# Performance work log

Hardware: AMD Instinct MI355X
Metric: run time of the kernel (lower is better)

The kernel has to match this reference:

```python
import jax, jax.numpy as jnp
import numpy as np

C = 256
HEADS = 8
HD = C // HEADS
WS = 7
SCALE = HD ** -0.5
EPS = 1e-5


def _ln(x, g, b):
    m = jnp.mean(x, axis=-1, keepdims=True)
    v = jnp.var(x, axis=-1, keepdims=True)
    return (x - m) * jax.lax.rsqrt(v + EPS) * g + b


def setup_inputs() -> dict:
    key = jax.random.key(0)
    ks = jax.random.split(key, 8)
    B, H, W = 32, 56, 56
    N = H * W
    hid = 4 * C
    s = lambda fan: 1.0 / np.sqrt(fan)
    return {
        "x": jax.random.normal(ks[0], (B, N, C), dtype=jnp.float32),
        "ln1_g": jnp.ones((C,), jnp.float32),
        "ln1_b": jnp.zeros((C,), jnp.float32),
        "qkv_w": jax.random.normal(ks[1], (C, 3 * C), jnp.float32) * s(C),
        "qkv_b": jnp.zeros((3 * C,), jnp.float32),
        "ln2_g": jnp.ones((C,), jnp.float32),
        "ln2_b": jnp.zeros((C,), jnp.float32),
        "fc1_w": jax.random.normal(ks[2], (C, hid), jnp.float32) * s(C),
        "fc1_b": jnp.zeros((hid,), jnp.float32),
        "mlp_ln_g": jnp.ones((hid,), jnp.float32),
        "mlp_ln_b": jnp.zeros((hid,), jnp.float32),
        "fc2_w": jax.random.normal(ks[3], (hid, C), jnp.float32) * s(hid),
        "fc2_b": jnp.zeros((C,), jnp.float32),
        "H": H,
        "W": W,
    }


def _lsa(x, qkv_w, qkv_b, H, W):
    # x: (B, N, C); H, W divisible by WS -> padding is zero (matches torch path)
    B, N, _ = x.shape
    hp, wp = H // WS, W // WS
    P = hp * wp
    # window partition: (B, P, WS*WS, C)
    xw = x.reshape(B, hp, WS, wp, WS, C).transpose(0, 1, 3, 2, 4, 5).reshape(B, P, WS * WS, C)
    qkv = xw @ qkv_w + qkv_b                      # (B, P, 49, 3C)
    qkv = qkv.reshape(B, P, WS * WS, 3, HEADS, HD).transpose(3, 0, 1, 4, 2, 5)
    q, k, v = qkv[0], qkv[1], qkv[2]              # (B, P, heads, 49, HD)
    attn = jax.nn.softmax(jnp.einsum('bphqd,bphkd->bphqk', q * SCALE, k), axis=-1)
    out = jnp.einsum('bphqk,bphkd->bphqd', attn, v)
    # merge heads, un-window: note LSA never applies self.proj (faithful)
    out = out.transpose(0, 1, 3, 2, 4).reshape(B, hp, wp, WS, WS, C)
    out = out.transpose(0, 1, 3, 2, 4, 5).reshape(B, N, C)
    return out


def reference(x, ln1_g, ln1_b, qkv_w, qkv_b, ln2_g, ln2_b,
              fc1_w, fc1_b, mlp_ln_g, mlp_ln_b, fc2_w, fc2_b, H, W):
    x = x + _lsa(_ln(x, ln1_g, ln1_b), qkv_w, qkv_b, H, W)
    h = _ln(x, ln2_g, ln2_b)
    h = jax.nn.gelu(h @ fc1_w + fc1_b, approximate=False)
    h = _ln(h, mlp_ln_g, mlp_ln_b)
    x = x + (h @ fc2_w + fc2_b)
    return x
```

## Files before the change

### kernel.cpp

```cpp
#include <hip/hip_runtime.h>
#include <cmath>

typedef __bf16 bf16;
typedef __bf16 bf16x4 __attribute__((ext_vector_type(4)));
typedef __bf16 bf16x8 __attribute__((ext_vector_type(8)));
typedef float floatx4 __attribute__((ext_vector_type(4)));

constexpr int BATCH = 32;
constexpr int NTOK  = 3136;
constexpr int CDIM  = 256;
constexpr int MROWS = BATCH * NTOK;
constexpr int HIDD  = 1024;
constexpr float ATTN_SCALE = 0.17677669529663689f;

__device__ __forceinline__ float gelu_fast(float x) {
    float p = fmaf(0.044715f * x, x * x, x);
    return __fdividef(x, 1.0f + __expf(-1.5957691216057308f * p));
}

__device__ __forceinline__ void load8(const bf16* p, float* o) {
    bf16x8 v = *reinterpret_cast<const bf16x8*>(p);
#pragma unroll
    for (int j = 0; j < 8; j++) o[j] = (float)v[j];
}

__device__ __forceinline__ void gload_lds16(const void* g, void* l) {
    __builtin_amdgcn_global_load_lds(
        (const __attribute__((address_space(1))) void*)g,
        (__attribute__((address_space(3))) void*)l, 16, 0, 0);
}

__global__ __launch_bounds__(256) void wt_kernel(
    const float* __restrict__ Win, bf16* __restrict__ Wt, int Ksz, int Nsz,
    const float* __restrict__ gsc, int swz)
{
    int id = blockIdx.x * 256 + threadIdx.x;
    int n = id / Ksz, k = id % Ksz;
    float v = Win[(size_t)k * Nsz + n];
    if (gsc) v *= gsc[k];
    int kp = k ^ (swz & ((n & 7) << 3));
    Wt[(size_t)n * Ksz + kp] = (bf16)v;
}

__global__ __launch_bounds__(256) void c12_part_kernel(
    const float* __restrict__ W, const float* __restrict__ g,
    const float* __restrict__ b, float2* __restrict__ part)
{
    int n = threadIdx.x, j = blockIdx.x;
    float c1 = 0.f, c2 = 0.f;
#pragma unroll 8
    for (int k = j * 64; k < j * 64 + 64; k++) {
        float w = W[(size_t)k * 256 + n];
        c1 = fmaf(b[k], w, c1);
        c2 = fmaf(g[k], w, c2);
    }
    part[j * 256 + n] = make_float2(c1, c2);
}

__global__ __launch_bounds__(256) void c12_red_kernel(
    const float2* __restrict__ part, float2* __restrict__ c12)
{
    int n = threadIdx.x;
    float c1 = 0.f, c2 = 0.f;
#pragma unroll
    for (int j = 0; j < 16; j++) { float2 p = part[j * 256 + n]; c1 += p.x; c2 += p.y; }
    c12[n] = make_float2(c1, c2);
}

__global__ __launch_bounds__(256) void ln_apply_f32_kernel(
    const float* __restrict__ X, const float* __restrict__ g,
    const float* __restrict__ b, bf16* __restrict__ Y, int swz)
{
    int tok  = (blockIdx.x * 256 + threadIdx.x) >> 6;
    int lane = threadIdx.x & 63;
    const float* row = X + (size_t)tok * CDIM;
    float4 v = *reinterpret_cast<const float4*>(row + lane * 4);
    float s  = v.x + v.y + v.z + v.w;
    float ss = v.x * v.x + v.y * v.y + v.z * v.z + v.w * v.w;
#pragma unroll
    for (int off = 32; off > 0; off >>= 1) {
        s  += __shfl_xor(s,  off, 64);
        ss += __shfl_xor(ss, off, 64);
    }
    float mean = s * (1.0f / CDIM);
    float var  = ss * (1.0f / CDIM) - mean * mean;
    if (var < 0.f) var = 0.f;
    float rstd = rsqrtf(var + 1e-5f);
    float4 gg = *reinterpret_cast<const float4*>(g + lane * 4);
    float4 bb = *reinterpret_cast<const float4*>(b + lane * 4);
    bf16x4 o;
    o[0] = (bf16)((v.x - mean) * rstd * gg.x + bb.x);
    o[1] = (bf16)((v.y - mean) * rstd * gg.y + bb.y);
    o[2] = (bf16)((v.z - mean) * rstd * gg.z + bb.z);
    o[3] = (bf16)((v.w - mean) * rstd * gg.w + bb.w);
    int off4 = (lane * 4) ^ (swz & ((tok & 7) << 3));
    *reinterpret_cast<bf16x4*>(Y + (size_t)tok * CDIM + off4) = o;
}

__global__ __launch_bounds__(256) void ln_inplace_h_kernel(
    bf16* __restrict__ H, const float* __restrict__ g, const float* __restrict__ b)
{
    int tok  = (blockIdx.x * 256 + threadIdx.x) >> 6;
    int lane = threadIdx.x & 63;
    bf16* row = H + (size_t)tok * HIDD;
    float f[16];
    load8(row + lane * 8, f);
    load8(row + 512 + lane * 8, f + 8);
    float s = 0.f, ss = 0.f;
#pragma unroll
    for (int j = 0; j < 16; j++) { s += f[j]; ss += f[j] * f[j]; }
#pragma unroll
    for (int off = 32; off > 0; off >>= 1) {
        s  += __shfl_xor(s,  off, 64);
        ss += __shfl_xor(ss, off, 64);
    }
    float mean = s * (1.0f / HIDD);
    float var  = ss * (1.0f / HIDD) - mean * mean;
    if (var < 0.f) var = 0.f;
    float rstd = rsqrtf(var + 1e-5f);
    bf16x8 o0, o1;
#pragma unroll
    for (int j = 0; j < 8; j++) {
        o0[j] = (bf16)((f[j]     - mean) * rstd * g[lane * 8 + j]       + b[lane * 8 + j]);
        o1[j] = (bf16)((f[j + 8] - mean) * rstd * g[512 + lane * 8 + j] + b[512 + lane * 8 + j]);
    }
    *reinterpret_cast<bf16x8*>(row + lane * 8) = o0;
    *reinterpret_cast<bf16x8*>(row + 512 + lane * 8) = o1;
}

template<int EPI, bool SWZ, typename TO>
__global__ __launch_bounds__(256) void gemm_bt_kernel(
    const bf16* __restrict__ A, const bf16* __restrict__ Bt,
    const float* __restrict__ bias, const float* __restrict__ resid,
    TO* __restrict__ out, int Nsz, int Ksz)
{
    __shared__ bf16 lA[128 * 64];
    __shared__ bf16 lB[128 * 64];
    const int t = threadIdx.x;
    const int lane = t & 63, w = t >> 6;
    const int quad = lane >> 4, l16 = lane & 15;
    const int wm = (w >> 1) * 64, wn = (w & 1) * 64;

    const int gx   = gridDim.x;
    const int flat = blockIdx.y * gx + blockIdx.x;
    const int cpx  = (gx * gridDim.y) >> 3;
    const int fl2  = (flat & 7) * cpx + (flat >> 3);
    const int bx   = fl2 % gx, by = fl2 / gx;

    const size_t m0 = (size_t)by * 128;
    const int n0 = bx * 128;
    const int srow = w * 32 + (lane >> 3);
    const int scol = (lane & 7) * 8;
    const int swzr = SWZ ? ((l16 & 7) << 3) : 0;

    floatx4 acc[4][4] = {};

    for (int kc = 0; kc < Ksz; kc += 64) {
#pragma unroll
        for (int j = 0; j < 4; j++) {
            gload_lds16(A  + (m0 + srow + j * 8) * Ksz + kc + scol, &lA[(w * 32 + j * 8) * 64]);
            gload_lds16(Bt + (size_t)(n0 + srow + j * 8) * Ksz + kc + scol, &lB[(w * 32 + j * 8) * 64]);
        }
        __syncthreads();
#pragma unroll
        for (int ks = 0; ks < 64; ks += 32) {
            bf16x8 af[4], bfv[4];
#pragma unroll
            for (int i = 0; i < 4; i++) {
                af[i]  = *reinterpret_cast<const bf16x8*>(&lA[(wm + i * 16 + l16) * 64 + ((ks + quad * 8) ^ swzr)]);
                bfv[i] = *reinterpret_cast<const bf16x8*>(&lB[(wn + i * 16 + l16) * 64 + ((ks + quad * 8) ^ swzr)]);
            }
#pragma unroll
            for (int mi = 0; mi < 4; mi++)
#pragma unroll
                for (int ni = 0; ni < 4; ni++)
                    acc[mi][ni] = __builtin_amdgcn_mfma_f32_16x16x32_bf16(af[mi], bfv[ni], acc[mi][ni], 0, 0, 0);
        }
        __syncthreads();
    }

#pragma unroll
    for (int mi = 0; mi < 4; mi++) {
#pragma unroll
        for (int ni = 0; ni < 4; ni++) {
            int col = n0 + wn + ni * 16 + l16;
            float bcol = bias[col];
#pragma unroll
            for (int r = 0; r < 4; r++) {
                size_t row = m0 + wm + mi * 16 + quad * 4 + r;
                float v = acc[mi][ni][r] + bcol;
                if (EPI == 1) v = gelu_fast(v);
                if (EPI == 3) v += resid[row * (size_t)Nsz + col];
                out[row * (size_t)Nsz + col] = (TO)v;
            }
        }
    }
}

__global__ __launch_bounds__(256, 2) void mlp_fused_kernel(
    const bf16* __restrict__ A,
    const bf16* __restrict__ W1t,
    const bf16* __restrict__ W2t,
    const float* __restrict__ b1, const float* __restrict__ b2,
    const float* __restrict__ resid, const float2* __restrict__ c12,
    float* __restrict__ out)
{
    __shared__ bf16 lP[24576];
    __shared__ bf16 lH[64 * 128];
    __shared__ float2 lstats[64][2];

    const int t = threadIdx.x;
    const int lane = t & 63, w = t >> 6;
    const int quad = lane >> 4, l16 = lane & 15;
    const int whid  = (w >> 1) * 64, wtok1 = (w & 1) * 32;
    const int wtok2 = (w >> 1) * 32, wout  = (w & 1) * 128;

    const int cpx = gridDim.x >> 3;
    const int bid = (blockIdx.x & 7) * cpx + (blockIdx.x >> 3);
    const size_t m0 = (size_t)bid * 64;

    const int srow  = t >> 4;
    const int schk  = (t & 15) * 8;
    const int lrow  = lane >> 3;
    const int scol  = (lane & 7) * 8;
    const int swzr  = (l16 & 7) << 3;

    bf16* lX  = lP;
    bf16* lW1 = lP + 8192;
    bf16* lW2 = lP;

    floatx4 acc2[2][8] = {};
    float tsum[2] = {0.f, 0.f};
    float tss[2]  = {0.f, 0.f};

    for (int nc = 0; nc < 8; nc++) {
        floatx4 sT[4][2] = {};
#pragma unroll
        for (int kc2 = 0; kc2 < 2; kc2++) {
            const int kc = kc2 * 128;
#pragma unroll
            for (int j = 0; j < 4; j++)
                gload_lds16(A + (m0 + j * 16 + srow) * 256 + kc + schk,
                            &lX[(j * 16 + w * 4) * 128]);
#pragma unroll
            for (int j = 0; j < 8; j++)
                gload_lds16(W1t + (size_t)(nc * 128 + j * 16 + srow) * 256 + kc + schk,
                            &lW1[(j * 16 + w * 4) * 128]);
            __syncthreads();
#pragma unroll
            for (int ks = 0; ks < 128; ks += 32) {
                bf16x8 wf[4], xf[2];
#pragma unroll
                for (int i = 0; i < 4; i++)
                    wf[i] = *reinterpret_cast<const bf16x8*>(&lW1[(whid + i * 16 + l16) * 128 + ((ks + quad * 8) ^ swzr)]);
#pragma unroll
                for (int i = 0; i < 2; i++)
                    xf[i] = *reinterpret_cast<const bf16x8*>(&lX[(wtok1 + i * 16 + l16) * 128 + ((ks + quad * 8) ^ swzr)]);
#pragma unroll
                for (int mt = 0; mt < 4; mt++)
#pragma unroll
                    for (int nt = 0; nt < 2; nt++)
                        sT[mt][nt] = __builtin_amdgcn_mfma_f32_16x16x32_bf16(wf[mt], xf[nt], sT[mt][nt], 0, 0, 0);
            }
            __syncthreads();
        }
#pragma unroll
        for (int mt = 0; mt < 4; mt++) {
            float4 b1v = *reinterpret_cast<const float4*>(&b1[nc * 128 + whid + mt * 16 + quad * 4]);
            const float* b1p = reinterpret_cast<const float*>(&b1v);
#pragma unroll
            for (int nt = 0; nt < 2; nt++) {
                bf16x4 h4;
#pragma unroll
                for (int r = 0; r < 4; r++) {
                    float v = gelu_fast(sT[mt][nt][r] + b1p[r]);
                    tsum[nt] += v;
                    tss[nt] = fmaf(v, v, tss[nt]);
                    h4[r] = (bf16)v;
                }
                int tok  = wtok1 + nt * 16 + l16;
                int hidb = (whid + mt * 16 + quad * 4) ^ swzr;
                *reinterpret_cast<bf16x4*>(&lH[tok * 128 + hidb]) = h4;
            }
        }
        __syncthreads();
#pragma unroll
        for (int k2s = 0; k2s < 2; k2s++) {
#pragma unroll
            for (int j = 0; j < 8; j++)
                gload_lds16(W2t + (size_t)(w * 64 + j * 8 + lrow) * 1024
                                + nc * 128 + k2s * 64 + scol,
                            &lW2[(w * 64 + j * 8) * 64]);
            __syncthreads();
#pragma unroll
            for (int ks2 = 0; ks2 < 64; ks2 += 32) {
                bf16x8 hf[2];
#pragma unroll
                for (int i = 0; i < 2; i++)
                    hf[i] = *reinterpret_cast<const bf16x8*>(
                        &lH[(wtok2 + i * 16 + l16) * 128 + ((k2s * 64 + ks2 + quad * 8) ^ swzr)]);
#pragma unroll
                for (int g4 = 0; g4 < 2; g4++) {
                    bf16x8 vf[4];
#pragma unroll
                    for (int i = 0; i < 4; i++)
                        vf[i] = *reinterpret_cast<const bf16x8*>(
                            &lW2[(wout + (g4 * 4 + i) * 16 + l16) * 64 + ((ks2 + quad * 8) ^ swzr)]);
#pragma unroll
                    for (int mi = 0; mi < 2; mi++)
#pragma unroll
                        for (int i = 0; i < 4; i++)
                            acc2[mi][g4 * 4 + i] = __builtin_amdgcn_mfma_f32_16x16x32_bf16(
                                hf[mi], vf[i], acc2[mi][g4 * 4 + i], 0, 0, 0);
                }
            }
            __syncthreads();
        }
    }

#pragma unroll
    for (int nt = 0; nt < 2; nt++) {
        float s = tsum[nt], ss = tss[nt];
        s  += __shfl_xor(s, 16, 64);  ss += __shfl_xor(ss, 16, 64);
        s  += __shfl_xor(s, 32, 64);  ss += __shfl_xor(ss, 32, 64);
        if (quad == 0) lstats[wtok1 + nt * 16 + l16][w >> 1] = make_float2(s, ss);
    }
    __syncthreads();

    float bcol[8]; float2 cc[8];
#pragma unroll
    for (int ni = 0; ni < 8; ni++) {
        int col = wout + ni * 16 + l16;
        bcol[ni] = b2[col];
        cc[ni] = c12[col];
    }
#pragma unroll
    for (int mi = 0; mi < 2; mi++) {
#pragma unroll
        for (int r = 0; r < 4; r++) {
            int rl = wtok2 + mi * 16 + quad * 4 + r;
            float2 p0 = lstats[rl][0], p1 = lstats[rl][1];
            float s = p0.x + p1.x, ss = p0.y + p1.y;
            float mean = s * (1.0f / HIDD);
            float var  = ss * (1.0f / HIDD) - mean * mean;
            if (var < 0.f) var = 0.f;
            float rstd = rsqrtf(var + 1e-5f);
            float ofs = -mean * rstd;
            size_t row = m0 + rl;
            const float* rr = resid + row * CDIM;
            float* orow = out + row * CDIM;
#pragma unroll
            for (int ni = 0; ni < 8; ni++) {
                int col = wout + ni * 16 + l16;
                float v = fmaf(rstd, acc2[mi][ni][r], fmaf(ofs, cc[ni].y, cc[ni].x + bcol[ni]));
                orow[col] = v + rr[col];
            }
        }
    }
}

__global__ __launch_bounds__(256) void attn_kernel(
    const bf16* __restrict__ qkv, const float* __restrict__ X,
    float* __restrict__ x1)
{
    __shared__ bf16 pbuf[4][64 * 72];
    __shared__ bf16 vtbuf[4][32 * 72];
    const int w = threadIdx.x >> 6, lane = threadIdx.x & 63;
    const int quad = lane >> 4, l16 = lane & 15;
    const int blk = blockIdx.x;
    const int hg = blk & 1, p = (blk >> 1) & 63, b = blk >> 7;
    const int h = hg * 4 + w;
    const int py = p >> 3, px = p & 7;
    const size_t gbase = (size_t)b * NTOK + py * 7 * 56 + px * 7;
    bf16* P  = pbuf[w];
    bf16* VT = vtbuf[w];

    unsigned int* vz = (unsigned int*)VT;
    for (int i = lane; i < 32 * 72 / 2; i += 64) vz[i] = 0u;

    for (int idx = lane; idx < 49 * 4; idx += 64) {
        int tk = idx >> 2, d8 = (idx & 3) * 8;
        size_t g = gbase + (tk / 7) * 56 + (tk % 7);
        bf16x8 vv = *reinterpret_cast<const bf16x8*>(qkv + g * 768 + 512 + h * 32 + d8);
#pragma unroll
        for (int j = 0; j < 8; j++) VT[(d8 + j) * 72 + tk] = vv[j];
    }

    bf16x8 qf[4], kf[4];
#pragma unroll
    for (int mt = 0; mt < 4; mt++) {
        int i = mt * 16 + l16; if (i > 48) i = 48;
        size_t g = gbase + (i / 7) * 56 + (i % 7);
        qf[mt] = *reinterpret_cast<const bf16x8*>(qkv + g * 768 +       h * 32 + quad * 8);
        kf[mt] = *reinterpret_cast<const bf16x8*>(qkv + g * 768 + 256 + h * 32 + quad * 8);
    }

    floatx4 s[4][4];
#pragma unroll
    for (int mt = 0; mt < 4; mt++)
#pragma unroll
        for (int nt = 0; nt < 4; nt++) {
            floatx4 z = {};
            s[mt][nt] = __builtin_amdgcn_mfma_f32_16x16x32_bf16(qf[mt], kf[nt], z, 0, 0, 0);
        }

#pragma unroll
    for (int mt = 0; mt < 4; mt++) {
#pragma unroll
        for (int r = 0; r < 4; r++) {
            float mx = -1e30f;
#pragma unroll
            for (int nt = 0; nt < 4; nt++) {
                int col = nt * 16 + l16;
                float v = (col < 49) ? s[mt][nt][r] * ATTN_SCALE : -1e30f;
                s[mt][nt][r] = v;
                mx = fmaxf(mx, v);
            }
#pragma unroll
            for (int off = 1; off < 16; off <<= 1) mx = fmaxf(mx, __shfl_xor(mx, off, 64));
            float sum = 0.f;
#pragma unroll
            for (int nt = 0; nt < 4; nt++) {
                float e = __expf(s[mt][nt][r] - mx);
                s[mt][nt][r] = e;
                sum += e;
            }
#pragma unroll
            for (int off = 1; off < 16; off <<= 1) sum += __shfl_xor(sum, off, 64);
            float inv = 1.0f / sum;
            int prow = mt * 16 + quad * 4 + r;
#pragma unroll
            for (int nt = 0; nt < 4; nt++)
                P[prow * 72 + nt * 16 + l16] = (bf16)(s[mt][nt][r] * inv);
        }
    }

    __syncthreads();

    floatx4 o[4][2] = {};
#pragma unroll
    for (int ks = 0; ks < 2; ks++) {
        bf16x8 pf[4], vf[2];
#pragma unroll
        for (int mt = 0; mt < 4; mt++)
            pf[mt] = *reinterpret_cast<const bf16x8*>(&P[(mt * 16 + l16) * 72 + ks * 32 + quad * 8]);
#pragma unroll
        for (int nt = 0; nt < 2; nt++)
            vf[nt] = *reinterpret_cast<const bf16x8*>(&VT[(nt * 16 + l16) * 72 + ks * 32 + quad * 8]);
#pragma unroll
        for (int mt = 0; mt < 4; mt++)
#pragma unroll
            for (int nt = 0; nt < 2; nt++)
                o[mt][nt] = __builtin_amdgcn_mfma_f32_16x16x32_bf16(pf[mt], vf[nt], o[mt][nt], 0, 0, 0);
    }

#pragma unroll
    for (int mt = 0; mt < 4; mt++) {
#pragma unroll
        for (int r = 0; r < 4; r++) {
            int i = mt * 16 + quad * 4 + r;
            if (i < 49) {
                size_t g = gbase + (i / 7) * 56 + (i % 7);
#pragma unroll
                for (int nt = 0; nt < 2; nt++) {
                    size_t adr = g * CDIM + h * 32 + nt * 16 + l16;
                    x1[adr] = X[adr] + o[mt][nt][r];
                }
            }
        }
    }
}

extern "C" void kernel_launch(void* const* d_in, const int* in_sizes, int n_in,
                              void* d_out, int out_size, void* d_ws, size_t ws_size,
                              hipStream_t stream) {
    const float* x      = (const float*)d_in[0];
    const float* ln1_g  = (const float*)d_in[1];
    const float* ln1_b  = (const float*)d_in[2];
    const float* qkv_w  = (const float*)d_in[3];
    const float* qkv_b  = (const float*)d_in[4];
    const float* ln2_g  = (const float*)d_in[5];
    const float* ln2_b  = (const float*)d_in[6];
    const float* fc1_w  = (const float*)d_in[7];
    const float* fc1_b  = (const float*)d_in[8];
    const float* mlp_g  = (const float*)d_in[9];
    const float* mlp_b  = (const float*)d_in[10];
    const float* fc2_w  = (const float*)d_in[11];
    const float* fc2_b  = (const float*)d_in[12];
    float* out = (float*)d_out;

    char* ws = (char*)d_ws;
    bf16* qkv_wt = (bf16*)ws;  ws += (size_t)768 * 256 * 2;
    bf16* fc1_wt = (bf16*)ws;  ws += (size_t)1024 * 256 * 2;
    bf16* fc2_wt = (bf16*)ws;  ws += (size_t)256 * 1024 * 2;
    bf16* xn     = (bf16*)ws;  ws += (size_t)MROWS * CDIM * 2;
    bf16* qkvb   = (bf16*)ws;
    bf16* hbuf   = (bf16*)ws;  ws += (size_t)MROWS * HIDD * 2;

    const size_t base_bytes = (size_t)(ws - (char*)d_ws);
    const size_t tail_bytes = (size_t)16 * 256 * sizeof(float2) + (size_t)256 * sizeof(float2);
    const bool fuse = (ws_size >= base_bytes + tail_bytes);
    const int swz = fuse ? 0x38 : 0;

    float2* c12p = (float2*)ws;
    float2* c12  = c12p + 16 * 256;
    float* x1 = out;

    wt_kernel<<<768,  256, 0, stream>>>(qkv_w, qkv_wt, 256, 768, nullptr, swz);
    wt_kernel<<<1024, 256, 0, stream>>>(fc1_w, fc1_wt, 256, 1024, nullptr, swz);
    wt_kernel<<<1024, 256, 0, stream>>>(fc2_w, fc2_wt, 1024, 256,
                                        fuse ? mlp_g : nullptr, swz);
    if (fuse) {
        c12_part_kernel<<<16, 256, 0, stream>>>(fc2_w, mlp_g, mlp_b, c12p);
        c12_red_kernel<<<1, 256, 0, stream>>>(c12p, c12);
    }

    ln_apply_f32_kernel<<<MROWS / 4, 256, 0, stream>>>(x, ln1_g, ln1_b, xn, swz);
    if (fuse)
        gemm_bt_kernel<0, true, bf16><<<dim3(768 / 128, MROWS / 128), 256, 0, stream>>>(
            xn, qkv_wt, qkv_b, nullptr, qkvb, 768, 256);
    else
        gemm_bt_kernel<0, false, bf16><<<dim3(768 / 128, MROWS / 128), 256, 0, stream>>>(
            xn, qkv_wt, qkv_b, nullptr, qkvb, 768, 256);
    attn_kernel<<<BATCH * 64 * 2, 256, 0, stream>>>(qkvb, x, x1);
    ln_apply_f32_kernel<<<MROWS / 4, 256, 0, stream>>>(x1, ln2_g, ln2_b, xn, swz);

    if (fuse) {
        mlp_fused_kernel<<<MROWS / 64, 256, 0, stream>>>(
            xn, fc1_wt, fc2_wt, fc1_b, fc2_b, x1, c12, out);
    } else {
        gemm_bt_kernel<1, false, bf16><<<dim3(HIDD / 128, MROWS / 128), 256, 0, stream>>>(
            xn, fc1_wt, fc1_b, nullptr, hbuf, HIDD, 256);
        ln_inplace_h_kernel<<<MROWS / 4, 256, 0, stream>>>(hbuf, mlp_g, mlp_b);
        gemm_bt_kernel<3, false, float><<<dim3(CDIM / 128, MROWS / 128), 256, 0, stream>>>(
            hbuf, fc2_wt, fc2_b, x1, out, CDIM, 1024);
    }
}
```

Before: 638.6 us.

## Load MLP weights directly from global memory and keep X tile resident in LDS

The fused MLP kernel now loads the full 64x256 activation tile into LDS once, instead of reloading it for each of the 8 hidden chunks. W1 and W2 fragments are read straight from global memory into registers rather than staged through LDS. This removes many LDS stores and block barriers per chunk, and the fc1/fc2 weight transposes are now written unswizzled to match. In exchange, every wave issues uncached-layout global loads for weights, which depends on L2/L1 hit rates and may add latency that the barriers previously hid.

```diff
diff --git a/kernel.cpp b/kernel.cpp
--- a/kernel.cpp
+++ b/kernel.cpp
@@ -205,7 +205,7 @@
     const float* __restrict__ resid, const float2* __restrict__ c12,
     float* __restrict__ out)
 {
-    __shared__ bf16 lP[24576];
+    __shared__ bf16 lX[64 * 256];
     __shared__ bf16 lH[64 * 128];
     __shared__ float2 lstats[64][2];
 
@@ -219,15 +219,13 @@
     const int bid = (blockIdx.x & 7) * cpx + (blockIdx.x >> 3);
     const size_t m0 = (size_t)bid * 64;
 
-    const int srow  = t >> 4;
-    const int schk  = (t & 15) * 8;
-    const int lrow  = lane >> 3;
-    const int scol  = (lane & 7) * 8;
-    const int swzr  = (l16 & 7) << 3;
-
-    bf16* lX  = lP;
-    bf16* lW1 = lP + 8192;
-    bf16* lW2 = lP;
+    const int swzr = (l16 & 7) << 3;
+
+#pragma unroll
+    for (int j = 0; j < 8; j++)
+        gload_lds16(A + (m0 + j * 8 + (t >> 5)) * 256 + (t & 31) * 8,
+                    &lX[j * 2048 + w * 512]);
+    __syncthreads();
 
     floatx4 acc2[2][8] = {};
     float tsum[2] = {0.f, 0.f};
@@ -235,35 +233,25 @@
 
     for (int nc = 0; nc < 8; nc++) {
         floatx4 sT[4][2] = {};
-#pragma unroll
-        for (int kc2 = 0; kc2 < 2; kc2++) {
-            const int kc = kc2 * 128;
-#pragma unroll
-            for (int j = 0; j < 4; j++)
-                gload_lds16(A + (m0 + j * 16 + srow) * 256 + kc + schk,
-                            &lX[(j * 16 + w * 4) * 128]);
-#pragma unroll
-            for (int j = 0; j < 8; j++)
-                gload_lds16(W1t + (size_t)(nc * 128 + j * 16 + srow) * 256 + kc + schk,
-                            &lW1[(j * 16 + w * 4) * 128]);
-            __syncthreads();
-#pragma unroll
-            for (int ks = 0; ks < 128; ks += 32) {
-                bf16x8 wf[4], xf[2];
-#pragma unroll
-                for (int i = 0; i < 4; i++)
-                    wf[i] = *reinterpret_cast<const bf16x8*>(&lW1[(whid + i * 16 + l16) * 128 + ((ks + quad * 8) ^ swzr)]);
-#pragma unroll
-                for (int i = 0; i < 2; i++)
-                    xf[i] = *reinterpret_cast<const bf16x8*>(&lX[(wtok1 + i * 16 + l16) * 128 + ((ks + quad * 8) ^ swzr)]);
-#pragma unroll
-                for (int mt = 0; mt < 4; mt++)
-#pragma unroll
-                    for (int nt = 0; nt < 2; nt++)
-                        sT[mt][nt] = __builtin_amdgcn_mfma_f32_16x16x32_bf16(wf[mt], xf[nt], sT[mt][nt], 0, 0, 0);
-            }
-            __syncthreads();
-        }
+        const bf16* w1base = W1t + (size_t)(nc * 128) * 256;
+#pragma unroll
+        for (int ks = 0; ks < 256; ks += 32) {
+            bf16x8 wf[4], xf[2];
+#pragma unroll
+            for (int i = 0; i < 4; i++)
+                wf[i] = *reinterpret_cast<const bf16x8*>(
+                    w1base + (size_t)(whid + i * 16 + l16) * 256 + ks + quad * 8);
+#pragma unroll
+            for (int i = 0; i < 2; i++)
+                xf[i] = *reinterpret_cast<const bf16x8*>(
+                    &lX[(wtok1 + i * 16 + l16) * 256 + ((ks + quad * 8) ^ swzr)]);
+#pragma unroll
+            for (int mt = 0; mt < 4; mt++)
+#pragma unroll
+                for (int nt = 0; nt < 2; nt++)
+                    sT[mt][nt] = __builtin_amdgcn_mfma_f32_16x16x32_bf16(wf[mt], xf[nt], sT[mt][nt], 0, 0, 0);
+        }
+        __syncthreads();
 #pragma unroll
         for (int mt = 0; mt < 4; mt++) {
             float4 b1v = *reinterpret_cast<const float4*>(&b1[nc * 128 + whid + mt * 16 + quad * 4]);
@@ -285,36 +273,27 @@
         }
         __syncthreads();
 #pragma unroll
-        for (int k2s = 0; k2s < 2; k2s++) {
-#pragma unroll
-            for (int j = 0; j < 8; j++)
-                gload_lds16(W2t + (size_t)(w * 64 + j * 8 + lrow) * 1024
-                                + nc * 128 + k2s * 64 + scol,
-                            &lW2[(w * 64 + j * 8) * 64]);
-            __syncthreads();
-#pragma unroll
-            for (int ks2 = 0; ks2 < 64; ks2 += 32) {
-                bf16x8 hf[2];
-#pragma unroll
-                for (int i = 0; i < 2; i++)
-                    hf[i] = *reinterpret_cast<const bf16x8*>(
-                        &lH[(wtok2 + i * 16 + l16) * 128 + ((k2s * 64 + ks2 + quad * 8) ^ swzr)]);
-#pragma unroll
-                for (int g4 = 0; g4 < 2; g4++) {
-                    bf16x8 vf[4];
+        for (int ks2 = 0; ks2 < 128; ks2 += 32) {
+            bf16x8 hf[2];
+#pragma unroll
+            for (int i = 0; i < 2; i++)
+                hf[i] = *reinterpret_cast<const bf16x8*>(
+                    &lH[(wtok2 + i * 16 + l16) * 128 + ((ks2 + quad * 8) ^ swzr)]);
+#pragma unroll
+            for (int g4 = 0; g4 < 2; g4++) {
+                bf16x8 vf[4];
+#pragma unroll
+                for (int i = 0; i < 4; i++)
+                    vf[i] = *reinterpret_cast<const bf16x8*>(
+                        W2t + (size_t)(wout + (g4 * 4 + i) * 16 + l16) * 1024
+                            + nc * 128 + ks2 + quad * 8);
+#pragma unroll
+                for (int mi = 0; mi < 2; mi++)
 #pragma unroll
                     for (int i = 0; i < 4; i++)
-                        vf[i] = *reinterpret_cast<const bf16x8*>(
-                            &lW2[(wout + (g4 * 4 + i) * 16 + l16) * 64 + ((ks2 + quad * 8) ^ swzr)]);
-#pragma unroll
-                    for (int mi = 0; mi < 2; mi++)
-#pragma unroll
-                        for (int i = 0; i < 4; i++)
-                            acc2[mi][g4 * 4 + i] = __builtin_amdgcn_mfma_f32_16x16x32_bf16(
-                                hf[mi], vf[i], acc2[mi][g4 * 4 + i], 0, 0, 0);
-                }
-            }
-            __syncthreads();
+                        acc2[mi][g4 * 4 + i] = __builtin_amdgcn_mfma_f32_16x16x32_bf16(
+                            hf[mi], vf[i], acc2[mi][g4 * 4 + i], 0, 0, 0);
+            }
         }
     }
 
@@ -507,9 +486,9 @@
     float* x1 = out;
 
     wt_kernel<<<768,  256, 0, stream>>>(qkv_w, qkv_wt, 256, 768, nullptr, swz);
-    wt_kernel<<<1024, 256, 0, stream>>>(fc1_w, fc1_wt, 256, 1024, nullptr, swz);
+    wt_kernel<<<1024, 256, 0, stream>>>(fc1_w, fc1_wt, 256, 1024, nullptr, 0);
     wt_kernel<<<1024, 256, 0, stream>>>(fc2_w, fc2_wt, 1024, 256,
-                                        fuse ? mlp_g : nullptr, swz);
+                                        fuse ? mlp_g : nullptr, 0);
     if (fuse) {
         c12_part_kernel<<<16, 256, 0, stream>>>(fc2_w, mlp_g, mlp_b, c12p);
         c12_red_kernel<<<1, 256, 0, stream>>>(c12p, c12);
```

Measured after the change: 959.2 us. 50.2% more time.
